# Kernel tuning notes

Measured on AMD Instinct MI355X. Metric: run time of the kernel, lower is better.

Reference implementation:

```python
import jax, jax.numpy as jnp
import numpy as np

N_NODES = 50000
N_EDGES = 800000
D = 128
LN_EPS = 1e-5


def setup_inputs() -> dict:
    key = jax.random.key(0)
    ks = jax.random.split(key, 6)
    x = jax.random.normal(ks[0], (N_NODES, D), dtype=jnp.float32)
    edge_index = jax.random.randint(ks[1], (2, N_EDGES), 0, N_NODES, dtype=jnp.int32)
    # MeanAggregator.linear: (D -> D)
    agg_W = jax.random.normal(ks[2], (D, D), dtype=jnp.float32) / np.sqrt(D)
    agg_b = jnp.zeros((D,), dtype=jnp.float32)
    # GraphSAGELayer.linear: (2D -> D)
    W = jax.random.normal(ks[3], (2 * D, D), dtype=jnp.float32) / np.sqrt(2 * D)
    b = jnp.zeros((D,), dtype=jnp.float32)
    gamma = jnp.ones((D,), dtype=jnp.float32)
    beta = jnp.zeros((D,), dtype=jnp.float32)
    return {"x": x, "edge_index": edge_index, "agg_W": agg_W, "agg_b": agg_b,
            "W": W, "b": b, "gamma": gamma, "beta": beta}


def reference(x, edge_index, agg_W, agg_b, W, b, gamma, beta):
    row, col = edge_index[0], edge_index[1]
    num_nodes = x.shape[0]
    # mean aggregation: scatter-add source features x[row] into destination col
    nbr_sum = jax.ops.segment_sum(x[row], col, num_segments=num_nodes)  # [N, D]
    deg = jax.ops.segment_sum(jnp.ones_like(col, dtype=x.dtype), col,
                              num_segments=num_nodes)
    deg = jnp.clip(deg, 1.0)
    aggregated = nbr_sum / deg[:, None]
    agg_features = aggregated @ agg_W + agg_b  # MeanAggregator.linear
    combined = jnp.concatenate([x, agg_features], axis=-1)  # [N, 2D]
    out = jax.nn.relu(combined @ W + b)
    # LayerNorm over last dim
    mu = jnp.mean(out, axis=-1, keepdims=True)
    var = jnp.var(out, axis=-1, keepdims=True)
    out = (out - mu) * jax.lax.rsqrt(var + LN_EPS) * gamma + beta
    # dropout: inference mode -> identity
    return out
```

## Files before the change

### kernel.cpp

```cpp
#include <hip/hip_runtime.h>

#define N_NODES 50000
#define N_EDGES 800000
#define D_FEAT 128
#define LN_EPS 1e-5f
#define TM 64
#define CVT_B 3125
#define NBUCK 391
#define BCAP 3072
#define BIN1_E 4096
#define BIN1_B 196

typedef __attribute__((ext_vector_type(8))) short bf16x8;
typedef __attribute__((ext_vector_type(4))) float f32x4;

__device__ __forceinline__ unsigned short f2bf(float f) {
    union { float f; unsigned int i; } v; v.f = f;
    unsigned int x = v.i;
    unsigned int lsb = (x >> 16) & 1u;
    x += 0x7fffu + lsb;
    return (unsigned short)(x >> 16);
}
__device__ __forceinline__ float bflo(unsigned int u) {
    union { unsigned int i; float f; } v; v.i = u << 16; return v.f;
}
__device__ __forceinline__ float bfhi(unsigned int u) {
    union { unsigned int i; float f; } v; v.i = u & 0xffff0000u; return v.f;
}
__device__ __forceinline__ int clampn(int v) {
    return (v < 0) ? 0 : ((v >= N_NODES) ? (N_NODES - 1) : v);
}
__device__ __forceinline__ void split2(float f0, float f1,
                                       unsigned int& hp, unsigned int& lp) {
    unsigned short h0 = f2bf(f0), h1 = f2bf(f1);
    unsigned short l0 = f2bf(f0 - bflo(h0)), l1 = f2bf(f1 - bflo(h1));
    hp = ((unsigned)h1 << 16) | h0;
    lp = ((unsigned)l1 << 16) | l0;
}

__global__ void prep_kernel(const float* __restrict__ x,
                            const float* __restrict__ agg_W,
                            const float* __restrict__ agg_b,
                            const float* __restrict__ W,
                            const float* __restrict__ b,
                            uint4* __restrict__ AH4,
                            uint4* __restrict__ AL4,
                            unsigned short* __restrict__ Wt2h,
                            unsigned short* __restrict__ Wt2l,
                            float* __restrict__ cvec)
{
    int blk = blockIdx.x;
    if (blk < CVT_B) {
        int i = blk * 256 + threadIdx.x;
        const float4 a = *(const float4*)(x + (size_t)i * 8);
        const float4 c = *(const float4*)(x + (size_t)i * 8 + 4);
        uint4 h, l;
        split2(a.x, a.y, h.x, l.x);
        split2(a.z, a.w, h.y, l.y);
        split2(c.x, c.y, h.z, l.z);
        split2(c.z, c.w, h.w, l.w);
        size_t idx = (size_t)(i >> 4) * 32 + (i & 15);
        AH4[idx] = h;
        AL4[idx] = l;
    } else {
        int t = blk - CVT_B;
        int n = threadIdx.x;
        if (n < 128) {
            float w1 = W[t * 128 + n];
            unsigned short h1 = f2bf(w1);
            Wt2h[n * 256 + t] = h1;
            Wt2l[n * 256 + t] = f2bf(w1 - bflo(h1));
            float m = 0.0f;
            for (int j = 0; j < 128; ++j)
                m += agg_W[t * 128 + j] * W[(128 + j) * 128 + n];
            unsigned short h2 = f2bf(m);
            Wt2h[n * 256 + 128 + t] = h2;
            Wt2l[n * 256 + 128 + t] = f2bf(m - bflo(h2));
            if (t == 0) {
                float s = b[n];
                for (int j = 0; j < 128; ++j)
                    s += agg_b[j] * W[(128 + j) * 128 + n];
                cvec[n] = s;
            }
        }
    }
}

__global__ __launch_bounds__(512) void binpass1_kernel(const int* __restrict__ ei,
                                                       unsigned int* __restrict__ bcurs,
                                                       unsigned int* __restrict__ binned)
{
    __shared__ int esrc[BIN1_E];
    __shared__ unsigned short edst[BIN1_E];
    __shared__ int hist[NBUCK];
    __shared__ unsigned int cur2[NBUCK];
    int t    = threadIdx.x;
    int base = blockIdx.x * BIN1_E;

    for (int i = t; i < NBUCK; i += 512) hist[i] = 0;
    #pragma unroll
    for (int i = 0; i < BIN1_E / 512; ++i) {
        int idx = i * 512 + t;
        int e = base + idx;
        if (e < N_EDGES) {
            esrc[idx] = clampn(ei[e]);
            edst[idx] = (unsigned short)clampn(ei[N_EDGES + e]);
        } else {
            esrc[idx] = -1;
        }
    }
    __syncthreads();

    #pragma unroll
    for (int i = 0; i < BIN1_E / 512; ++i) {
        int idx = i * 512 + t;
        if (esrc[idx] >= 0) atomicAdd(&hist[(int)edst[idx] >> 7], 1);
    }
    __syncthreads();

    for (int bk = t; bk < NBUCK; bk += 512) {
        int c = hist[bk];
        unsigned int off = c ? atomicAdd(&bcurs[bk], (unsigned int)c) : 0u;
        cur2[bk] = (unsigned int)bk * BCAP + off;
    }
    __syncthreads();

    #pragma unroll
    for (int i = 0; i < BIN1_E / 512; ++i) {
        int idx = i * 512 + t;
        int src = esrc[idx];
        if (src >= 0) {
            int dst = (int)edst[idx];
            int bk  = dst >> 7;
            unsigned int slot = atomicAdd(&cur2[bk], 1u);
            if (slot < (unsigned int)bk * BCAP + BCAP)
                binned[slot] = (unsigned int)src | ((unsigned int)dst << 16);
        }
    }
}

__global__ __launch_bounds__(512) void binpass2_kernel(const unsigned int* __restrict__ binned,
                                                       const unsigned int* __restrict__ bcurs,
                                                       int* __restrict__ pos,
                                                       int* __restrict__ deg_cnt,
                                                       unsigned short* __restrict__ edge_src)
{
    __shared__ int lscan[128];
    __shared__ int lcnt[128];
    __shared__ int lcur[128];
    int bk = blockIdx.x, t = threadIdx.x;

    unsigned int cnt = bcurs[bk]; if (cnt > BCAP) cnt = BCAP;
    unsigned int start = (unsigned int)bk * BCAP;
    unsigned int end   = start + cnt;

    int n0 = bk << 7;
    int nn = N_NODES - n0; if (nn > 128) nn = 128;

    if (t < 128) lcnt[t] = 0;
    __syncthreads();
    for (unsigned int e = start + t; e < end; e += 512)
        atomicAdd(&lcnt[(int)(binned[e] >> 16) & 127], 1);
    __syncthreads();

    int lv = (t < 128) ? lcnt[t] : 0;
    if (t < 128) lscan[t] = lv;
    __syncthreads();
    for (int off = 1; off < 128; off <<= 1) {
        int u = (t >= off && t < 128) ? lscan[t - off] : 0;
        __syncthreads();
        if (t < 128) lscan[t] += u;
        __syncthreads();
    }
    if (t < 128) {
        int ls = (int)start + lscan[t] - lv;
        lcur[t] = ls;
        if (t < nn) {
            pos[n0 + t]     = ls + lv;
            deg_cnt[n0 + t] = lv;
        }
    }
    __syncthreads();

    for (unsigned int e = start + t; e < end; e += 512) {
        unsigned int v = binned[e];
        int slot = atomicAdd(&lcur[(int)(v >> 16) & 127], 1);
        edge_src[slot] = (unsigned short)(v & 0xffffu);
    }
}

__global__ void gather_kernel(uint4* __restrict__ AH4,
                              uint4* __restrict__ AL4,
                              const int* __restrict__ pos,
                              const int* __restrict__ deg_cnt,
                              const unsigned short* __restrict__ edge_src)
{
    int tid  = threadIdx.x;
    int node = blockIdx.x * 4 + (tid >> 6);
    int lane = tid & 63;
    int quarter = lane >> 4;
    int sub     = lane & 15;
    if (node >= N_NODES) return;

    int end   = pos[node];
    int dcnt  = deg_cnt[node];
    int start = end - dcnt;

    float a0 = 0.f, a1 = 0.f, a2 = 0.f, a3 = 0.f,
          a4 = 0.f, a5 = 0.f, a6 = 0.f, a7 = 0.f;

    for (int b = start; b < end; b += 64) {
        int nb = end - b; if (nb > 64) nb = 64;
        int sid = (b + lane < end) ? (int)edge_src[b + lane] : 0;
        for (int j = 0; j < nb; j += 4) {
            int eidx = j + quarter;
            int s = __shfl(sid, eidx, 64);
            if (eidx < nb) {
                const uint4 v = AH4[(size_t)s * 32 + sub];
                a0 += bflo(v.x); a1 += bfhi(v.x);
                a2 += bflo(v.y); a3 += bfhi(v.y);
                a4 += bflo(v.z); a5 += bfhi(v.z);
                a6 += bflo(v.w); a7 += bfhi(v.w);
            }
        }
    }
    #pragma unroll
    for (int m = 16; m <= 32; m <<= 1) {
        a0 += __shfl_xor(a0, m, 64); a1 += __shfl_xor(a1, m, 64);
        a2 += __shfl_xor(a2, m, 64); a3 += __shfl_xor(a3, m, 64);
        a4 += __shfl_xor(a4, m, 64); a5 += __shfl_xor(a5, m, 64);
        a6 += __shfl_xor(a6, m, 64); a7 += __shfl_xor(a7, m, 64);
    }
    if (quarter == 0) {
        float inv = 1.0f / (float)((dcnt > 1) ? dcnt : 1);
        uint4 h, l;
        split2(a0 * inv, a1 * inv, h.x, l.x);
        split2(a2 * inv, a3 * inv, h.y, l.y);
        split2(a4 * inv, a5 * inv, h.z, l.z);
        split2(a6 * inv, a7 * inv, h.w, l.w);
        size_t idx = (size_t)node * 32 + 16 + sub;
        AH4[idx] = h;
        AL4[idx] = l;
    }
}

__global__ __launch_bounds__(256) void gsage_main(
        const unsigned short* __restrict__ AH,
        const unsigned short* __restrict__ AL,
        const unsigned short* __restrict__ Wt2h,
        const unsigned short* __restrict__ Wt2l,
        const float* __restrict__ cvec,
        const float* __restrict__ gamma,
        const float* __restrict__ beta,
        float* __restrict__ out)
{
    __shared__ unsigned short Bh[128][72];
    __shared__ unsigned short Bl[128][72];
    __shared__ float Sred[2][64][2];

    int tid  = threadIdx.x;
    int lane = tid & 63;
    int w    = tid >> 6;
    int wr   = w >> 1, wc = w & 1;
    int l15  = lane & 15, grp = lane >> 4;
    int node0 = blockIdx.x * TM;

    int scol  = tid >> 1;
    int spart = tid & 1;
    const uint4* srcH = (const uint4*)Wt2h + scol * 32 + spart * 4;
    const uint4* srcL = (const uint4*)Wt2l + scol * 32 + spart * 4;
    uint4* dstH = (uint4*)&Bh[scol][spart * 32];
    uint4* dstL = (uint4*)&Bl[scol][spart * 32];

    f32x4 acc[2][4];
    #pragma unroll
    for (int m = 0; m < 2; ++m)
        #pragma unroll
        for (int nf = 0; nf < 4; ++nf)
            acc[m][nf] = (f32x4){0.f, 0.f, 0.f, 0.f};

    int row0 = node0 + wr * 32 + l15;

    for (int c = 0; c < 4; ++c) {
        if (c) __syncthreads();
        #pragma unroll
        for (int j = 0; j < 4; ++j) {
            dstH[j] = srcH[c * 8 + j];
            dstL[j] = srcL[c * 8 + j];
        }
        __syncthreads();

        #pragma unroll
        for (int ks = 0; ks < 2; ++ks) {
            int krel = c * 64 + ks * 32 + grp * 8;

            bf16x8 ah[2], al[2];
            #pragma unroll
            for (int m = 0; m < 2; ++m) {
                int row = row0 + m * 16;
                if (row < N_NODES) {
                    ah[m] = *(const bf16x8*)(AH + (size_t)row * 256 + krel);
                    al[m] = *(const bf16x8*)(AL + (size_t)row * 256 + krel);
                } else {
                    ah[m] = (bf16x8){0,0,0,0,0,0,0,0};
                    al[m] = (bf16x8){0,0,0,0,0,0,0,0};
                }
            }

            #pragma unroll
            for (int nf = 0; nf < 4; ++nf) {
                int col = wc * 64 + nf * 16 + l15;
                bf16x8 bh = *(const bf16x8*)&Bh[col][ks * 32 + grp * 8];
                bf16x8 bl = *(const bf16x8*)&Bl[col][ks * 32 + grp * 8];
                #pragma unroll
                for (int m = 0; m < 2; ++m) {
                    acc[m][nf] = __builtin_amdgcn_mfma_f32_16x16x32_bf16(ah[m], bh, acc[m][nf], 0, 0, 0);
                    acc[m][nf] = __builtin_amdgcn_mfma_f32_16x16x32_bf16(al[m], bh, acc[m][nf], 0, 0, 0);
                    acc[m][nf] = __builtin_amdgcn_mfma_f32_16x16x32_bf16(ah[m], bl, acc[m][nf], 0, 0, 0);
                }
            }
        }
    }

    int colf0 = wc * 64 + l15;
    float cv[4], gv[4], bv[4];
    #pragma unroll
    for (int nf = 0; nf < 4; ++nf) {
        int col = colf0 + nf * 16;
        cv[nf] = cvec[col]; gv[nf] = gamma[col]; bv[nf] = beta[col];
    }

    #pragma unroll
    for (int m = 0; m < 2; ++m) {
        #pragma unroll
        for (int r = 0; r < 4; ++r) {
            float s1 = 0.f, s2 = 0.f;
            #pragma unroll
            for (int nf = 0; nf < 4; ++nf) {
                float v = acc[m][nf][r] + cv[nf];
                v = (v > 0.f) ? v : 0.f;
                acc[m][nf][r] = v;
                s1 += v; s2 += v * v;
            }
            #pragma unroll
            for (int msk = 1; msk < 16; msk <<= 1) {
                s1 += __shfl_xor(s1, msk, 64);
                s2 += __shfl_xor(s2, msk, 64);
            }
            if (l15 == 0) {
                int rl = wr * 32 + m * 16 + grp * 4 + r;
                Sred[wc][rl][0] = s1;
                Sred[wc][rl][1] = s2;
            }
        }
    }
    __syncthreads();

    #pragma unroll
    for (int m = 0; m < 2; ++m) {
        #pragma unroll
        for (int r = 0; r < 4; ++r) {
            int rl = wr * 32 + m * 16 + grp * 4 + r;
            float t1 = Sred[0][rl][0] + Sred[1][rl][0];
            float t2 = Sred[0][rl][1] + Sred[1][rl][1];
            float mu   = t1 * (1.0f / 128.0f);
            float var  = t2 * (1.0f / 128.0f) - mu * mu;
            float rstd = rsqrtf(var + LN_EPS);
            int node = node0 + rl;
            if (node < N_NODES) {
                #pragma unroll
                for (int nf = 0; nf < 4; ++nf)
                    out[(size_t)node * D_FEAT + colf0 + nf * 16] =
                        (acc[m][nf][r] - mu) * rstd * gv[nf] + bv[nf];
            }
        }
    }
}

extern "C" void kernel_launch(void* const* d_in, const int* in_sizes, int n_in,
                              void* d_out, int out_size, void* d_ws, size_t ws_size,
                              hipStream_t stream) {
    const float* x     = (const float*)d_in[0];
    const int*   ei    = (const int*)d_in[1];
    const float* agg_W = (const float*)d_in[2];
    const float* agg_b = (const float*)d_in[3];
    const float* W     = (const float*)d_in[4];
    const float* b     = (const float*)d_in[5];
    const float* gamma = (const float*)d_in[6];
    const float* beta  = (const float*)d_in[7];
    float*       out   = (float*)d_out;

    size_t out_bytes = (size_t)out_size * sizeof(float);

    if (n_in != 8)                       { hipMemsetAsync(d_out, 0x45, out_bytes, stream); return; }
    if (in_sizes[0] != N_NODES * D_FEAT) { hipMemsetAsync(d_out, 0x48, out_bytes, stream); return; }
    if (in_sizes[1] != 2 * N_EDGES)      { hipMemsetAsync(d_out, 0x49, out_bytes, stream); return; }
    if (out_size != N_NODES * D_FEAT)    { hipMemsetAsync(d_out, 0x47, out_bytes, stream); return; }

    int*   deg_cnt  = (int*)d_ws;
    int*   pos      = deg_cnt + N_NODES;
    unsigned short* edge_src = (unsigned short*)(pos + N_NODES);
    unsigned short* Wt2h = (unsigned short*)((int*)edge_src + N_EDGES);
    unsigned short* Wt2l = Wt2h + 128 * 256;
    float* cvec     = (float*)(Wt2l + 128 * 256);
    unsigned short* AH = (unsigned short*)(cvec + 128);
    unsigned short* AL = AH + (size_t)N_NODES * 256;
    size_t need_ws = ((size_t)N_NODES * 2 + N_EDGES + 256 * 128 + 128) * 4
                     + (size_t)N_NODES * 256 * 2 * 2;
    if (ws_size < need_ws)               { hipMemsetAsync(d_out, 0x46, out_bytes, stream); return; }

    unsigned int* binned = (unsigned int*)d_out;
    unsigned int* bcurs  = binned + (size_t)NBUCK * BCAP;

    hipMemsetAsync(bcurs, 0, NBUCK * sizeof(unsigned int), stream);
    prep_kernel<<<CVT_B + 128, 256, 0, stream>>>(
        x, agg_W, agg_b, W, b, (uint4*)AH, (uint4*)AL, Wt2h, Wt2l, cvec);
    binpass1_kernel<<<BIN1_B, 512, 0, stream>>>(ei, bcurs, binned);
    binpass2_kernel<<<NBUCK, 512, 0, stream>>>(binned, bcurs, pos, deg_cnt, edge_src);
    gather_kernel<<<(N_NODES + 3) / 4, 256, 0, stream>>>(
        (uint4*)AH, (uint4*)AL, pos, deg_cnt, edge_src);
    gsage_main<<<(N_NODES + TM - 1) / TM, 256, 0, stream>>>(
        AH, AL, Wt2h, Wt2l, cvec, gamma, beta, out);
}
```

Baseline: 183.9 us.

## Fuse edge binning into prep kernel and give each wave full output rows

```diff
diff --git a/kernel.cpp b/kernel.cpp
--- a/kernel.cpp
+++ b/kernel.cpp
@@ -4,7 +4,7 @@
 #define N_EDGES 800000
 #define D_FEAT 128
 #define LN_EPS 1e-5f
-#define TM 64
+#define TM 128
 #define CVT_B 3125
 #define NBUCK 391
 #define BCAP 3072
@@ -38,17 +38,26 @@
     lp = ((unsigned)l1 << 16) | l0;
 }
 
-__global__ void prep_kernel(const float* __restrict__ x,
-                            const float* __restrict__ agg_W,
-                            const float* __restrict__ agg_b,
-                            const float* __restrict__ W,
-                            const float* __restrict__ b,
-                            uint4* __restrict__ AH4,
-                            uint4* __restrict__ AL4,
-                            unsigned short* __restrict__ Wt2h,
-                            unsigned short* __restrict__ Wt2l,
-                            float* __restrict__ cvec)
+__global__ __launch_bounds__(256) void prep_kernel(
+        const float* __restrict__ x,
+        const int* __restrict__ ei,
+        const float* __restrict__ agg_W,
+        const float* __restrict__ agg_b,
+        const float* __restrict__ W,
+        const float* __restrict__ b,
+        uint4* __restrict__ AH4,
+        uint4* __restrict__ AL4,
+        unsigned int* __restrict__ bcurs,
+        unsigned int* __restrict__ binned,
+        unsigned short* __restrict__ Wt2h,
+        unsigned short* __restrict__ Wt2l,
+        float* __restrict__ cvec)
 {
+    __shared__ int esrc[BIN1_E];
+    __shared__ unsigned short edst[BIN1_E];
+    __shared__ int hist[NBUCK];
+    __shared__ unsigned int cur2[NBUCK];
+
     int blk = blockIdx.x;
     if (blk < CVT_B) {
         int i = blk * 256 + threadIdx.x;
@@ -62,8 +71,52 @@
         size_t idx = (size_t)(i >> 4) * 32 + (i & 15);
         AH4[idx] = h;
         AL4[idx] = l;
+    } else if (blk < CVT_B + BIN1_B) {
+        int t    = threadIdx.x;
+        int base = (blk - CVT_B) * BIN1_E;
+
+        for (int i = t; i < NBUCK; i += 256) hist[i] = 0;
+        #pragma unroll
+        for (int i = 0; i < BIN1_E / 256; ++i) {
+            int idx = i * 256 + t;
+            int e = base + idx;
+            if (e < N_EDGES) {
+                esrc[idx] = clampn(ei[e]);
+                edst[idx] = (unsigned short)clampn(ei[N_EDGES + e]);
+            } else {
+                esrc[idx] = -1;
+            }
+        }
+        __syncthreads();
+
+        #pragma unroll
+        for (int i = 0; i < BIN1_E / 256; ++i) {
+            int idx = i * 256 + t;
+            if (esrc[idx] >= 0) atomicAdd(&hist[(int)edst[idx] >> 7], 1);
+        }
+        __syncthreads();
+
+        for (int bk = t; bk < NBUCK; bk += 256) {
+            int c = hist[bk];
+            unsigned int off = c ? atomicAdd(&bcurs[bk], (unsigned int)c) : 0u;
+            cur2[bk] = (unsigned int)bk * BCAP + off;
+        }
+        __syncthreads();
+
+        #pragma unroll
+        for (int i = 0; i < BIN1_E / 256; ++i) {
+            int idx = i * 256 + t;
+            int src = esrc[idx];
+            if (src >= 0) {
+                int dst = (int)edst[idx];
+                int bk  = dst >> 7;
+                unsigned int slot = atomicAdd(&cur2[bk], 1u);
+                if (slot < (unsigned int)bk * BCAP + BCAP)
+                    binned[slot] = (unsigned int)src | ((unsigned int)dst << 16);
+            }
+        }
     } else {
-        int t = blk - CVT_B;
+        int t = blk - CVT_B - BIN1_B;
         int n = threadIdx.x;
         if (n < 128) {
             float w1 = W[t * 128 + n];
@@ -86,59 +139,6 @@
     }
 }
 
-__global__ __launch_bounds__(512) void binpass1_kernel(const int* __restrict__ ei,
-                                                       unsigned int* __restrict__ bcurs,
-                                                       unsigned int* __restrict__ binned)
-{
-    __shared__ int esrc[BIN1_E];
-    __shared__ unsigned short edst[BIN1_E];
-    __shared__ int hist[NBUCK];
-    __shared__ unsigned int cur2[NBUCK];
-    int t    = threadIdx.x;
-    int base = blockIdx.x * BIN1_E;
-
-    for (int i = t; i < NBUCK; i += 512) hist[i] = 0;
-    #pragma unroll
-    for (int i = 0; i < BIN1_E / 512; ++i) {
-        int idx = i * 512 + t;
-        int e = base + idx;
-        if (e < N_EDGES) {
-            esrc[idx] = clampn(ei[e]);
-            edst[idx] = (unsigned short)clampn(ei[N_EDGES + e]);
-        } else {
-            esrc[idx] = -1;
-        }
-    }
-    __syncthreads();
-
-    #pragma unroll
-    for (int i = 0; i < BIN1_E / 512; ++i) {
-        int idx = i * 512 + t;
-        if (esrc[idx] >= 0) atomicAdd(&hist[(int)edst[idx] >> 7], 1);
-    }
-    __syncthreads();
-
-    for (int bk = t; bk < NBUCK; bk += 512) {
-        int c = hist[bk];
-        unsigned int off = c ? atomicAdd(&bcurs[bk], (unsigned int)c) : 0u;
-        cur2[bk] = (unsigned int)bk * BCAP + off;
-    }
-    __syncthreads();
-
-    #pragma unroll
-    for (int i = 0; i < BIN1_E / 512; ++i) {
-        int idx = i * 512 + t;
-        int src = esrc[idx];
-        if (src >= 0) {
-            int dst = (int)edst[idx];
-            int bk  = dst >> 7;
-            unsigned int slot = atomicAdd(&cur2[bk], 1u);
-            if (slot < (unsigned int)bk * BCAP + BCAP)
-                binned[slot] = (unsigned int)src | ((unsigned int)dst << 16);
-        }
-    }
-}
-
 __global__ __launch_bounds__(512) void binpass2_kernel(const unsigned int* __restrict__ binned,
                                                        const unsigned int* __restrict__ bcurs,
                                                        int* __restrict__ pos,
@@ -256,12 +256,10 @@
 {
     __shared__ unsigned short Bh[128][72];
     __shared__ unsigned short Bl[128][72];
-    __shared__ float Sred[2][64][2];
 
     int tid  = threadIdx.x;
     int lane = tid & 63;
     int w    = tid >> 6;
-    int wr   = w >> 1, wc = w & 1;
     int l15  = lane & 15, grp = lane >> 4;
     int node0 = blockIdx.x * TM;
 
@@ -272,14 +270,14 @@
     uint4* dstH = (uint4*)&Bh[scol][spart * 32];
     uint4* dstL = (uint4*)&Bl[scol][spart * 32];
 
-    f32x4 acc[2][4];
+    f32x4 acc[2][8];
     #pragma unroll
     for (int m = 0; m < 2; ++m)
         #pragma unroll
-        for (int nf = 0; nf < 4; ++nf)
+        for (int nf = 0; nf < 8; ++nf)
             acc[m][nf] = (f32x4){0.f, 0.f, 0.f, 0.f};
 
-    int row0 = node0 + wr * 32 + l15;
+    int row0 = node0 + w * 32 + l15;
 
     for (int c = 0; c < 4; ++c) {
         if (c) __syncthreads();
@@ -308,8 +306,8 @@
             }
 
             #pragma unroll
-            for (int nf = 0; nf < 4; ++nf) {
-                int col = wc * 64 + nf * 16 + l15;
+            for (int nf = 0; nf < 8; ++nf) {
+                int col = nf * 16 + l15;
                 bf16x8 bh = *(const bf16x8*)&Bh[col][ks * 32 + grp * 8];
                 bf16x8 bl = *(const bf16x8*)&Bl[col][ks * 32 + grp * 8];
                 #pragma unroll
@@ -322,11 +320,10 @@
         }
     }
 
-    int colf0 = wc * 64 + l15;
-    float cv[4], gv[4], bv[4];
+    float cv[8], gv[8], bv[8];
     #pragma unroll
-    for (int nf = 0; nf < 4; ++nf) {
-        int col = colf0 + nf * 16;
+    for (int nf = 0; nf < 8; ++nf) {
+        int col = nf * 16 + l15;
         cv[nf] = cvec[col]; gv[nf] = gamma[col]; bv[nf] = beta[col];
     }
 
@@ -336,7 +333,7 @@
         for (int r = 0; r < 4; ++r) {
             float s1 = 0.f, s2 = 0.f;
             #pragma unroll
-            for (int nf = 0; nf < 4; ++nf) {
+            for (int nf = 0; nf < 8; ++nf) {
                 float v = acc[m][nf][r] + cv[nf];
                 v = (v > 0.f) ? v : 0.f;
                 acc[m][nf][r] = v;
@@ -347,30 +344,14 @@
                 s1 += __shfl_xor(s1, msk, 64);
                 s2 += __shfl_xor(s2, msk, 64);
             }
-            if (l15 == 0) {
-                int rl = wr * 32 + m * 16 + grp * 4 + r;
-                Sred[wc][rl][0] = s1;
-                Sred[wc][rl][1] = s2;
-            }
-        }
-    }
-    __syncthreads();
-
-    #pragma unroll
-    for (int m = 0; m < 2; ++m) {
-        #pragma unroll
-        for (int r = 0; r < 4; ++r) {
-            int rl = wr * 32 + m * 16 + grp * 4 + r;
-            float t1 = Sred[0][rl][0] + Sred[1][rl][0];
-            float t2 = Sred[0][rl][1] + Sred[1][rl][1];
-            float mu   = t1 * (1.0f / 128.0f);
-            float var  = t2 * (1.0f / 128.0f) - mu * mu;
+            float mu   = s1 * (1.0f / 128.0f);
+            float var  = s2 * (1.0f / 128.0f) - mu * mu;
             float rstd = rsqrtf(var + LN_EPS);
-            int node = node0 + rl;
+            int node = node0 + w * 32 + m * 16 + grp * 4 + r;
             if (node < N_NODES) {
                 #pragma unroll
-                for (int nf = 0; nf < 4; ++nf)
-                    out[(size_t)node * D_FEAT + colf0 + nf * 16] =
+                for (int nf = 0; nf < 8; ++nf)
+                    out[(size_t)node * D_FEAT + nf * 16 + l15] =
                         (acc[m][nf][r] - mu) * rstd * gv[nf] + bv[nf];
             }
         }
@@ -413,9 +394,9 @@
     unsigned int* bcurs  = binned + (size_t)NBUCK * BCAP;
 
     hipMemsetAsync(bcurs, 0, NBUCK * sizeof(unsigned int), stream);
-    prep_kernel<<<CVT_B + 128, 256, 0, stream>>>(
-        x, agg_W, agg_b, W, b, (uint4*)AH, (uint4*)AL, Wt2h, Wt2l, cvec);
-    binpass1_kernel<<<BIN1_B, 512, 0, stream>>>(ei, bcurs, binned);
+    prep_kernel<<<CVT_B + BIN1_B + 128, 256, 0, stream>>>(
+        x, ei, agg_W, agg_b, W, b, (uint4*)AH, (uint4*)AL, bcurs, binned,
+        Wt2h, Wt2l, cvec);
     binpass2_kernel<<<NBUCK, 512, 0, stream>>>(binned, bcurs, pos, deg_cnt, edge_src);
     gather_kernel<<<(N_NODES + 3) / 4, 256, 0, stream>>>(
         (uint4*)AH, (uint4*)AL, pos, deg_cnt, edge_src);
```

Result: faster. 172.8 us, median of 2 (-6.0%).
